# Kernel optimization log

Measured on AMD Instinct MI355X. Metric: run time of the kernel, lower is better.

The kernel has to match this reference:

```python
import jax, jax.numpy as jnp
import numpy as np
import math

SR = 96000.0
FRAME = 2048
NB = 16
GAIN_RANGE = (-24.0, 24.0)
Q_RANGE = (0.5, 16.0)
BROADBAND = (-60.0, 0.0)
HPF_R = (20.0, 500.0)
LPF_R = (5000.0, 20000.0)
SHELF_R = (50.0, 16000.0)
PEAK_R = (100.0, 15000.0)


def _dfreq(n, rng):
    lo, hi = math.log(rng[0]), math.log(rng[1])
    return jnp.exp(lo + n * (hi - lo))


def _dgain(n, rng=GAIN_RANGE):
    return rng[0] + n * (rng[1] - rng[0])


def _dq(n):
    lo, hi = math.log(Q_RANGE[0]), math.log(Q_RANGE[1])
    return jnp.exp(lo + n * (hi - lo))


def _coeffs(ftype, fc, gain_db, Q):
    # returns stacked [g, k, a1, a2, a3, m0, m1, m2], each same shape as fc
    g = jnp.clip(jnp.tan(math.pi * fc / SR), 1e-6, 100.0)
    Q = jnp.clip(Q, 0.1, 100.0)
    one = jnp.ones_like(g)
    zero = jnp.zeros_like(g)
    if ftype in ('highpass', 'lowpass'):
        k = 1.0 / Q
        a1 = 1.0 / (1.0 + g * (g + k)); a2 = g * a1; a3 = g * a2
        if ftype == 'highpass':
            m0, m1, m2 = one, -k, -one
        else:
            m0, m1, m2 = zero, zero, one
    elif ftype == 'peak':
        A = jnp.power(10.0, gain_db / 40.0)
        k = jnp.where(gain_db >= 0, 1.0 / (Q * A), A / Q)
        a1 = 1.0 / (1.0 + g * (g + k)); a2 = g * a1; a3 = g * a2
        m0, m1, m2 = one, k * (A * A - 1.0), zero
    elif ftype == 'lowshelf':
        A = jnp.power(10.0, gain_db / 40.0); sA = jnp.sqrt(A); k = 1.0 / Q
        gs = jnp.where(gain_db >= 0, g / sA, g * sA)
        a1 = 1.0 / (1.0 + gs * (gs + k)); a2 = gs * a1; a3 = gs * a2
        m0, m1, m2 = one, k * (A - 1.0), A * A - 1.0
    else:  # highshelf
        A = jnp.power(10.0, gain_db / 40.0); sA = jnp.sqrt(A); k = 1.0 / Q
        gs = jnp.where(gain_db >= 0, g * sA, g / sA)
        a1 = 1.0 / (1.0 + gs * (gs + k)); a2 = gs * a1; a3 = gs * a2
        m0, m1, m2 = A * A, k * (1.0 - A) * A, 1.0 - A * A
    return jnp.stack([g, k, a1, a2, a3, m0, m1, m2], 0)


def _all_coeffs(params, n_frames_audio):
    # params: (B, 50, n_frames_params) -> coeffs (nF, NB, 8, B), in/out gains (nF, B)
    B = params.shape[0]
    nFp = params.shape[2]
    pidx = jnp.minimum(jnp.arange(n_frames_audio), nFp - 1)
    fp = jnp.take(params, pidx, axis=2)                 # (B, 50, nF)
    bq = fp[:, :NB * 3, :].reshape(B, NB, 3, n_frames_audio)
    in_g = jnp.power(10.0, _dgain(fp[:, -2, :], BROADBAND) / 20.0)   # (B, nF)
    out_g = jnp.power(10.0, _dgain(fp[:, -1, :], BROADBAND) / 20.0)  # (B, nF)
    cs = []
    for i in range(NB):
        fn, gn, qn = bq[:, i, 0], bq[:, i, 1], bq[:, i, 2]  # (B, nF)
        Q = _dq(qn)
        if i == 0:
            c = _coeffs('highpass', _dfreq(fn, HPF_R), None, Q)
        elif i == 15:
            c = _coeffs('lowpass', _dfreq(fn, LPF_R), None, Q)
        elif i == 1:
            c = _coeffs('lowshelf', _dfreq(fn, SHELF_R), _dgain(gn), Q)
        elif i == 14:
            c = _coeffs('highshelf', _dfreq(fn, SHELF_R), _dgain(gn), Q)
        else:
            c = _coeffs('peak', _dfreq(fn, PEAK_R), _dgain(gn), Q)
        cs.append(c)  # (8, B, nF)
    coeffs = jnp.transpose(jnp.stack(cs, 0), (3, 0, 1, 2))  # (nF, NB, 8, B)
    return coeffs, in_g.T, out_g.T


def _forward(audio, params):
    B, S = audio.shape
    nF = S // FRAME  # S chosen as exact multiple of FRAME
    coeffs, in_g, out_g = _all_coeffs(params, nF)
    frames = jnp.transpose(audio.reshape(B, nF, FRAME), (1, 2, 0))  # (nF, FRAME, B)

    def frame_step(states, xs):
        fr, c, ig, og = xs  # fr (FRAME,B), c (NB,8,B), ig (B,), og (B,)
        x = fr * ig[None, :]
        new_states = []
        for i in range(NB):
            a1, a2, a3 = c[i, 2], c[i, 3], c[i, 4]
            m0, m1, m2 = c[i, 5], c[i, 6], c[i, 7]

            def samp(st, xn, a1=a1, a2=a2, a3=a3, m0=m0, m1=m1, m2=m2):
                ic1, ic2 = st
                v3 = xn - ic2
                v1 = a1 * ic1 + a2 * v3
                v2 = ic2 + a2 * v1 + a3 * v3
                out = m0 * xn + m1 * v1 + m2 * v2
                return (2.0 * v1 - ic1, 2.0 * v2 - ic2), out

            (ic1, ic2), x = jax.lax.scan(samp, (states[i, 0], states[i, 1]), x)
            new_states.append(jnp.stack([ic1, ic2], 0))
        return jnp.stack(new_states, 0), x * og[None, :]

    init = jnp.zeros((NB, 2, B), audio.dtype)
    _, out = jax.lax.scan(frame_step, init, (frames, coeffs, in_g, out_g))
    return jnp.transpose(out, (2, 0, 1)).reshape(B, S)  # (B, S)


_forward_jit = jax.jit(_forward)


def setup_inputs() -> dict:
    key = jax.random.key(0)
    k1, k2 = jax.random.split(key)
    B, S, nFp = 32, 49152, 24  # 24 frames of 2048 samples
    audio = jax.random.normal(k1, (B, S), dtype=jnp.float32) * 0.1
    params = jax.random.uniform(k2, (B, 50, nFp), dtype=jnp.float32)
    return {'audio': audio, 'params': params}


def reference(audio, params):
    return _forward_jit(audio, params)
```

## Files before the change

kernel.cpp:

```cpp
#include <hip/hip_runtime.h>
#include <math.h>

#define NBATCH 32
#define S      49152
#define NF     24
#define NB     16
#define NBLK   4
#define CHUNK  16
#define NCH    768
#define NWAVE  12

__device__ __forceinline__ float clampf(float x, float lo, float hi) {
    return fminf(fmaxf(x, lo), hi);
}

#define FOREACH_S(OP) \
    OP(s00) OP(s01) OP(s02) OP(s03) OP(s04) OP(s05) OP(s06) OP(s07) \
    OP(s08) OP(s09) OP(s10) OP(s11) OP(s12) OP(s13) OP(s14) OP(s15)

#define DECL_S(x) float x;

#define STEPA(x) { \
    const float n1_ = fmaf(t00, ic1, fmaf(t01, ic2, b0 * (x))); \
    const float n2_ = fmaf(t10, ic1, fmaf(t11, ic2, b1 * (x))); \
    ic1 = n1_; ic2 = n2_; }

#define STEPC(x) { \
    const float y_  = fmaf(c0, ic1, fmaf(c1, ic2, c2 * (x))); \
    const float n1_ = fmaf(t00, ic1, fmaf(t01, ic2, b0 * (x))); \
    const float n2_ = fmaf(t10, ic1, fmaf(t11, ic2, b1 * (x))); \
    (x) = y_; ic1 = n1_; ic2 = n2_; }

__global__ __launch_bounds__(NCH, 3)
void biquad_chain_kernel(const float* __restrict__ audio,
                         const float* __restrict__ params,
                         float* __restrict__ out,
                         unsigned int* __restrict__ ws)
{
    __shared__ float sc[NB][NF][16];
    __shared__ float sgain[2][NF];
    __shared__ float4 saggM[NWAVE];
    __shared__ float  saggC[NWAVE][2];
    __shared__ float  sv[NWAVE][2];

    const int t       = threadIdx.x;
    const int xcd     = blockIdx.x & 7;
    const int slot_   = blockIdx.x >> 3;
    const int bt      = xcd * 4 + (slot_ & 3);
    const int quarter = slot_ >> 2;
    const int lane    = t & 63;
    const int wave    = t >> 6;
    const int frame   = quarter * 6 + (wave >> 1);

    if (t < NB * NF) {
        const int f  = t / NF;
        const int fr = t % NF;
        const float* P = params + (size_t)bt * 50 * NF;
        const float fn = P[(3 * f + 0) * NF + fr];
        const float gn = P[(3 * f + 1) * NF + fr];
        const float qn = P[(3 * f + 2) * NF + fr];

        float Q = __expf(-0.69314718f + qn * 3.4657359f);
        Q = clampf(Q, 0.1f, 100.0f);

        float lo, hi;
        int type;
        if      (f == 0)  { lo = 20.0f;   hi = 500.0f;   type = 0; }
        else if (f == 15) { lo = 5000.0f; hi = 20000.0f; type = 1; }
        else if (f == 1)  { lo = 50.0f;   hi = 16000.0f; type = 3; }
        else if (f == 14) { lo = 50.0f;   hi = 16000.0f; type = 4; }
        else              { lo = 100.0f;  hi = 15000.0f; type = 2; }

        const float fc = __expf(__logf(lo) + fn * (__logf(hi) - __logf(lo)));
        float g_ = __tanf((float)M_PI * fc / 96000.0f);
        g_ = clampf(g_, 1e-6f, 100.0f);
        const float gdb = -24.0f + 48.0f * gn;

        float a1, a2, a3, m0, m1, m2;
        if (type == 0 || type == 1) {
            const float k = 1.0f / Q;
            a1 = 1.0f / (1.0f + g_ * (g_ + k)); a2 = g_ * a1; a3 = g_ * a2;
            if (type == 0) { m0 = 1.0f; m1 = -k;   m2 = -1.0f; }
            else           { m0 = 0.0f; m1 = 0.0f; m2 = 1.0f;  }
        } else if (type == 2) {
            const float A = __expf(gdb * (2.30258509f / 40.0f));
            const float k = (gdb >= 0.0f) ? 1.0f / (Q * A) : A / Q;
            a1 = 1.0f / (1.0f + g_ * (g_ + k)); a2 = g_ * a1; a3 = g_ * a2;
            m0 = 1.0f; m1 = k * (A * A - 1.0f); m2 = 0.0f;
        } else {
            const float A  = __expf(gdb * (2.30258509f / 40.0f));
            const float sA = sqrtf(A);
            const float k  = 1.0f / Q;
            float gs;
            if (type == 3) gs = (gdb >= 0.0f) ? g_ / sA : g_ * sA;
            else           gs = (gdb >= 0.0f) ? g_ * sA : g_ / sA;
            a1 = 1.0f / (1.0f + gs * (gs + k)); a2 = gs * a1; a3 = gs * a2;
            if (type == 3) { m0 = 1.0f;  m1 = k * (A - 1.0f);      m2 = A * A - 1.0f; }
            else           { m0 = A * A; m1 = k * (1.0f - A) * A;  m2 = 1.0f - A * A; }
        }

        const float q2  = a2 * a2 + a3;
        const float t00 = 2.0f * a1 - 1.0f;
        const float t01 = -2.0f * a2;
        const float t10 = 2.0f * a1 * a2;
        const float t11 = 1.0f - 2.0f * q2;
        const float b0  = 2.0f * a2;
        const float b1  = 2.0f * q2;
        const float c0  = a1 * (m1 + m2 * a2);
        const float c1  = m2 * (1.0f - q2) - m1 * a2;
        const float c2  = m0 + m1 * a2 + m2 * q2;

        float u00 = t00, u01 = t01, u10 = t10, u11 = t11;
        #pragma unroll
        for (int i = 0; i < 4; i++) {
            const float n00 = u00 * u00 + u01 * u10;
            const float n01 = u00 * u01 + u01 * u11;
            const float n10 = u10 * u00 + u11 * u10;
            const float n11 = u10 * u01 + u11 * u11;
            u00 = n00; u01 = n01; u10 = n10; u11 = n11;
        }

        sc[f][fr][0] = t00; sc[f][fr][1] = t01; sc[f][fr][2] = t10; sc[f][fr][3] = t11;
        sc[f][fr][4] = b0;  sc[f][fr][5] = b1;  sc[f][fr][6] = c0;  sc[f][fr][7] = c1;
        sc[f][fr][8] = c2;  sc[f][fr][9] = u00; sc[f][fr][10] = u01; sc[f][fr][11] = u10;
        sc[f][fr][12] = u11;
    }
    if (t >= 384 && t < 384 + 2 * NF) {
        const int idx = t - 384;
        const int which = idx / NF;
        const int fr    = idx % NF;
        const float* P = params + (size_t)bt * 50 * NF;
        const float p  = P[(48 + which) * NF + fr];
        const float db = -60.0f + 60.0f * p;
        sgain[which][fr] = __expf(db * (2.30258509f / 20.0f));
    }
    __syncthreads();

    FOREACH_S(DECL_S)
    {
        const float ing = sgain[0][frame];
        const float* base = audio + (size_t)bt * S
                          + (size_t)(quarter * NCH + t) * CHUNK;
        float4 q;
        q = *(const float4*)(base +  0); s00 = q.x*ing; s01 = q.y*ing; s02 = q.z*ing; s03 = q.w*ing;
        q = *(const float4*)(base +  4); s04 = q.x*ing; s05 = q.y*ing; s06 = q.z*ing; s07 = q.w*ing;
        q = *(const float4*)(base +  8); s08 = q.x*ing; s09 = q.y*ing; s10 = q.z*ing; s11 = q.w*ing;
        q = *(const float4*)(base + 12); s12 = q.x*ing; s13 = q.y*ing; s14 = q.z*ing; s15 = q.w*ing;
    }

    #pragma unroll 1
    for (int f = 0; f < NB; f++) {
        const float4 q0 = *(const float4*)&sc[f][frame][0];
        const float4 q1 = *(const float4*)&sc[f][frame][4];
        const float4 q2 = *(const float4*)&sc[f][frame][8];
        const float  M11v = sc[f][frame][12];
        const float t00 = q0.x, t01 = q0.y, t10 = q0.z, t11 = q0.w;
        const float b0  = q1.x, b1  = q1.y, c0  = q1.z, c1  = q1.w;
        const float c2  = q2.x;

        float ic1 = 0.0f, ic2 = 0.0f;
        FOREACH_S(STEPA)

        float Md00 = q2.y, Md01 = q2.z, Md10 = q2.w, Md11 = M11v;
        float Ac0 = ic1, Ac1 = ic2;
        #pragma unroll
        for (int d = 1; d < 64; d <<= 1) {
            const float lc0 = __shfl_up(Ac0, d);
            const float lc1 = __shfl_up(Ac1, d);
            if (lane >= d) {
                Ac0 = fmaf(Md00, lc0, fmaf(Md01, lc1, Ac0));
                Ac1 = fmaf(Md10, lc0, fmaf(Md11, lc1, Ac1));
            }
            const float n00 = Md00 * Md00 + Md01 * Md10;
            const float n01 = Md00 * Md01 + Md01 * Md11;
            const float n10 = Md10 * Md00 + Md11 * Md10;
            const float n11 = Md10 * Md01 + Md11 * Md11;
            Md00 = n00; Md01 = n01; Md10 = n10; Md11 = n11;
        }

        if (lane == 63) {
            saggM[wave] = make_float4(Md00, Md01, Md10, Md11);
            saggC[wave][0] = Ac0; saggC[wave][1] = Ac1;
        }
        __syncthreads();

        const unsigned int tag = (unsigned int)(f + 1);
        unsigned int* stagebase = ws + ((bt * NB + f) * NBLK) * 8;

        if (wave == 0) {
            float G00 = 1.0f, G01 = 0.0f, G10 = 0.0f, G11 = 1.0f, Gc0 = 0.0f, Gc1 = 0.0f;
            if (lane < NWAVE) {
                const float4 m = saggM[lane];
                G00 = m.x; G01 = m.y; G10 = m.z; G11 = m.w;
                Gc0 = saggC[lane][0]; Gc1 = saggC[lane][1];
            }
            #pragma unroll
            for (int d = 1; d < 16; d <<= 1) {
                const float l00 = __shfl_up(G00, d);
                const float l01 = __shfl_up(G01, d);
                const float l10 = __shfl_up(G10, d);
                const float l11 = __shfl_up(G11, d);
                const float lc0 = __shfl_up(Gc0, d);
                const float lc1 = __shfl_up(Gc1, d);
                if (lane >= d && lane < NWAVE) {
                    const float n00 = G00 * l00 + G01 * l10;
                    const float n01 = G00 * l01 + G01 * l11;
                    const float n10 = G10 * l00 + G11 * l10;
                    const float n11 = G10 * l01 + G11 * l11;
                    const float nc0 = G00 * lc0 + G01 * lc1 + Gc0;
                    const float nc1 = G10 * lc0 + G11 * lc1 + Gc1;
                    G00 = n00; G01 = n01; G10 = n10; G11 = n11;
                    Gc0 = nc0; Gc1 = nc1;
                }
            }

            if (quarter < NBLK - 1 && lane == NWAVE - 1) {
                unsigned int* slot = stagebase + quarter * 8;
                float* dp = (float*)(slot + 1);
                __hip_atomic_store(&dp[0], G00, __ATOMIC_RELAXED, __HIP_MEMORY_SCOPE_AGENT);
                __hip_atomic_store(&dp[1], G01, __ATOMIC_RELAXED, __HIP_MEMORY_SCOPE_AGENT);
                __hip_atomic_store(&dp[2], G10, __ATOMIC_RELAXED, __HIP_MEMORY_SCOPE_AGENT);
                __hip_atomic_store(&dp[3], G11, __ATOMIC_RELAXED, __HIP_MEMORY_SCOPE_AGENT);
                __hip_atomic_store(&dp[4], Gc0, __ATOMIC_RELAXED, __HIP_MEMORY_SCOPE_AGENT);
                __hip_atomic_store(&dp[5], Gc1, __ATOMIC_RELAXED, __HIP_MEMORY_SCOPE_AGENT);
                __hip_atomic_store(slot, tag, __ATOMIC_RELEASE, __HIP_MEMORY_SCOPE_AGENT);
            }

            float P00 = __shfl_up(G00, 1);
            float P01 = __shfl_up(G01, 1);
            float P10 = __shfl_up(G10, 1);
            float P11 = __shfl_up(G11, 1);
            float Pc0 = __shfl_up(Gc0, 1);
            float Pc1 = __shfl_up(Gc1, 1);
            if (lane == 0) { P00 = 1.0f; P01 = 0.0f; P10 = 0.0f; P11 = 1.0f; Pc0 = 0.0f; Pc1 = 0.0f; }

            float S0x = 0.0f, S0y = 0.0f;
            if (lane == 0 && quarter > 0) {
                float sx = 0.0f, sy = 0.0f;
                for (int k2 = 0; k2 < quarter; k2++) {
                    unsigned int* slot = stagebase + k2 * 8;
                    while (__hip_atomic_load(slot, __ATOMIC_ACQUIRE, __HIP_MEMORY_SCOPE_AGENT) != tag) {
                        __builtin_amdgcn_s_sleep(1);
                    }
                    float* dp = (float*)(slot + 1);
                    const float m00 = __hip_atomic_load(&dp[0], __ATOMIC_RELAXED, __HIP_MEMORY_SCOPE_AGENT);
                    const float m01 = __hip_atomic_load(&dp[1], __ATOMIC_RELAXED, __HIP_MEMORY_SCOPE_AGENT);
                    const float m10 = __hip_atomic_load(&dp[2], __ATOMIC_RELAXED, __HIP_MEMORY_SCOPE_AGENT);
                    const float m11 = __hip_atomic_load(&dp[3], __ATOMIC_RELAXED, __HIP_MEMORY_SCOPE_AGENT);
                    const float cc0 = __hip_atomic_load(&dp[4], __ATOMIC_RELAXED, __HIP_MEMORY_SCOPE_AGENT);
                    const float cc1 = __hip_atomic_load(&dp[5], __ATOMIC_RELAXED, __HIP_MEMORY_SCOPE_AGENT);
                    const float nx = m00 * sx + m01 * sy + cc0;
                    const float ny = m10 * sx + m11 * sy + cc1;
                    sx = nx; sy = ny;
                }
                S0x = sx; S0y = sy;
            }
            S0x = __shfl(S0x, 0);
            S0y = __shfl(S0y, 0);

            if (lane < NWAVE) {
                sv[lane][0] = fmaf(P00, S0x, fmaf(P01, S0y, Pc0));
                sv[lane][1] = fmaf(P10, S0x, fmaf(P11, S0y, Pc1));
            }
        }
        __syncthreads();

        const float vx = sv[wave][0];
        const float vy = sv[wave][1];

        float ce0 = __shfl_up(Ac0, 1);
        float ce1 = __shfl_up(Ac1, 1);
        if (lane == 0) { ce0 = 0.0f; ce1 = 0.0f; }

        float w0 = vx, w1 = vy;
        float p00 = q2.y, p01 = q2.z, p10 = q2.w, p11 = M11v;
        #pragma unroll
        for (int b = 0; b < 6; b++) {
            if (lane & (1 << b)) {
                const float nw0 = fmaf(p00, w0, p01 * w1);
                const float nw1 = fmaf(p10, w0, p11 * w1);
                w0 = nw0; w1 = nw1;
            }
            if (b < 5) {
                const float n00 = p00 * p00 + p01 * p10;
                const float n01 = p00 * p01 + p01 * p11;
                const float n10 = p10 * p00 + p11 * p10;
                const float n11 = p10 * p01 + p11 * p11;
                p00 = n00; p01 = n01; p10 = n10; p11 = n11;
            }
        }
        ic1 = w0 + ce0;
        ic2 = w1 + ce1;

        FOREACH_S(STEPC)
    }

    {
        const float og = sgain[1][frame];
        float* base = out + (size_t)bt * S + (size_t)(quarter * NCH + t) * CHUNK;
        float4 q;
        q.x = s00*og; q.y = s01*og; q.z = s02*og; q.w = s03*og; *(float4*)(base +  0) = q;
        q.x = s04*og; q.y = s05*og; q.z = s06*og; q.w = s07*og; *(float4*)(base +  4) = q;
        q.x = s08*og; q.y = s09*og; q.z = s10*og; q.w = s11*og; *(float4*)(base +  8) = q;
        q.x = s12*og; q.y = s13*og; q.z = s14*og; q.w = s15*og; *(float4*)(base + 12) = q;
    }
}

extern "C" void kernel_launch(void* const* d_in, const int* in_sizes, int n_in,
                              void* d_out, int out_size, void* d_ws, size_t ws_size,
                              hipStream_t stream)
{
    const float* audio  = (const float*)d_in[0];
    const float* params = (const float*)d_in[1];
    float* out = (float*)d_out;
    unsigned int* ws = (unsigned int*)d_ws;
    biquad_chain_kernel<<<NBLK * NBATCH, NCH, 0, stream>>>(audio, params, out, ws);
}
```

Measured before the change: 125.3 us.

## Fuse biquad stages in pairs to halve parallel-scan and sync rounds

Result: slower. 204.6 us (+63.2%).

```diff
diff --git a/kernel.cpp b/kernel.cpp
--- a/kernel.cpp
+++ b/kernel.cpp
@@ -5,6 +5,7 @@
 #define S      49152
 #define NF     24
 #define NB     16
+#define NP     8
 #define NBLK   4
 #define CHUNK  16
 #define NCH    768
@@ -20,16 +21,82 @@
 
 #define DECL_S(x) float x;
 
-#define STEPA(x) { \
-    const float n1_ = fmaf(t00, ic1, fmaf(t01, ic2, b0 * (x))); \
-    const float n2_ = fmaf(t10, ic1, fmaf(t11, ic2, b1 * (x))); \
-    ic1 = n1_; ic2 = n2_; }
-
-#define STEPC(x) { \
-    const float y_  = fmaf(c0, ic1, fmaf(c1, ic2, c2 * (x))); \
-    const float n1_ = fmaf(t00, ic1, fmaf(t01, ic2, b0 * (x))); \
-    const float n2_ = fmaf(t10, ic1, fmaf(t11, ic2, b1 * (x))); \
-    (x) = y_; ic1 = n1_; ic2 = n2_; }
+#define STEPA2(x) { \
+    const float y1_  = fmaf(c0a, j1, fmaf(c1a, j2, c2a * (x))); \
+    const float nj1_ = fmaf(t00a, j1, fmaf(t01a, j2, b0a * (x))); \
+    const float nj2_ = fmaf(t10a, j1, fmaf(t11a, j2, b1a * (x))); \
+    const float nk1_ = fmaf(t00b, k1, fmaf(t01b, k2, b0b * y1_)); \
+    const float nk2_ = fmaf(t10b, k1, fmaf(t11b, k2, b1b * y1_)); \
+    j1 = nj1_; j2 = nj2_; k1 = nk1_; k2 = nk2_; }
+
+#define STEPC2(x) { \
+    const float y1_  = fmaf(c0a, j1, fmaf(c1a, j2, c2a * (x))); \
+    const float y2_  = fmaf(c0b, k1, fmaf(c1b, k2, c2b * y1_)); \
+    const float nj1_ = fmaf(t00a, j1, fmaf(t01a, j2, b0a * (x))); \
+    const float nj2_ = fmaf(t10a, j1, fmaf(t11a, j2, b1a * (x))); \
+    const float nk1_ = fmaf(t00b, k1, fmaf(t01b, k2, b0b * y1_)); \
+    const float nk2_ = fmaf(t10b, k1, fmaf(t11b, k2, b1b * y1_)); \
+    (x) = y2_; j1 = nj1_; j2 = nj2_; k1 = nk1_; k2 = nk2_; }
+
+struct Aff { float t00, t01, t10, t11, b0, b1, c0, c1, c2; };
+
+__device__ __forceinline__ Aff biquad_affine(int f, const float* P, int fr) {
+    const float fn = P[(3 * f + 0) * NF + fr];
+    const float gn = P[(3 * f + 1) * NF + fr];
+    const float qn = P[(3 * f + 2) * NF + fr];
+
+    float Q = __expf(-0.69314718f + qn * 3.4657359f);
+    Q = clampf(Q, 0.1f, 100.0f);
+
+    float lo, hi;
+    int type;
+    if      (f == 0)  { lo = 20.0f;   hi = 500.0f;   type = 0; }
+    else if (f == 15) { lo = 5000.0f; hi = 20000.0f; type = 1; }
+    else if (f == 1)  { lo = 50.0f;   hi = 16000.0f; type = 3; }
+    else if (f == 14) { lo = 50.0f;   hi = 16000.0f; type = 4; }
+    else              { lo = 100.0f;  hi = 15000.0f; type = 2; }
+
+    const float fc = __expf(__logf(lo) + fn * (__logf(hi) - __logf(lo)));
+    float g_ = __tanf((float)M_PI * fc / 96000.0f);
+    g_ = clampf(g_, 1e-6f, 100.0f);
+    const float gdb = -24.0f + 48.0f * gn;
+
+    float a1, a2, a3, m0, m1, m2;
+    if (type == 0 || type == 1) {
+        const float k = 1.0f / Q;
+        a1 = 1.0f / (1.0f + g_ * (g_ + k)); a2 = g_ * a1; a3 = g_ * a2;
+        if (type == 0) { m0 = 1.0f; m1 = -k;   m2 = -1.0f; }
+        else           { m0 = 0.0f; m1 = 0.0f; m2 = 1.0f;  }
+    } else if (type == 2) {
+        const float A = __expf(gdb * (2.30258509f / 40.0f));
+        const float k = (gdb >= 0.0f) ? 1.0f / (Q * A) : A / Q;
+        a1 = 1.0f / (1.0f + g_ * (g_ + k)); a2 = g_ * a1; a3 = g_ * a2;
+        m0 = 1.0f; m1 = k * (A * A - 1.0f); m2 = 0.0f;
+    } else {
+        const float A  = __expf(gdb * (2.30258509f / 40.0f));
+        const float sA = sqrtf(A);
+        const float k  = 1.0f / Q;
+        float gs;
+        if (type == 3) gs = (gdb >= 0.0f) ? g_ / sA : g_ * sA;
+        else           gs = (gdb >= 0.0f) ? g_ * sA : g_ / sA;
+        a1 = 1.0f / (1.0f + gs * (gs + k)); a2 = gs * a1; a3 = gs * a2;
+        if (type == 3) { m0 = 1.0f;  m1 = k * (A - 1.0f);      m2 = A * A - 1.0f; }
+        else           { m0 = A * A; m1 = k * (1.0f - A) * A;  m2 = 1.0f - A * A; }
+    }
+
+    const float q2 = a2 * a2 + a3;
+    Aff r;
+    r.t00 = 2.0f * a1 - 1.0f;
+    r.t01 = -2.0f * a2;
+    r.t10 = 2.0f * a1 * a2;
+    r.t11 = 1.0f - 2.0f * q2;
+    r.b0  = 2.0f * a2;
+    r.b1  = 2.0f * q2;
+    r.c0  = a1 * (m1 + m2 * a2);
+    r.c1  = m2 * (1.0f - q2) - m1 * a2;
+    r.c2  = m0 + m1 * a2 + m2 * q2;
+    return r;
+}
 
 __global__ __launch_bounds__(NCH, 3)
 void biquad_chain_kernel(const float* __restrict__ audio,
@@ -37,11 +104,10 @@
                          float* __restrict__ out,
                          unsigned int* __restrict__ ws)
 {
-    __shared__ float sc[NB][NF][16];
+    __shared__ float sc[NP][NF][32];
     __shared__ float sgain[2][NF];
-    __shared__ float4 saggM[NWAVE];
-    __shared__ float  saggC[NWAVE][2];
-    __shared__ float  sv[NWAVE][2];
+    __shared__ float sagg[NWAVE][16];
+    __shared__ float sv[NWAVE][4];
 
     const int t       = threadIdx.x;
     const int xcd     = blockIdx.x & 7;
@@ -52,78 +118,46 @@
     const int wave    = t >> 6;
     const int frame   = quarter * 6 + (wave >> 1);
 
-    if (t < NB * NF) {
-        const int f  = t / NF;
+    if (t < NP * NF) {
+        const int p  = t / NF;
         const int fr = t % NF;
         const float* P = params + (size_t)bt * 50 * NF;
-        const float fn = P[(3 * f + 0) * NF + fr];
-        const float gn = P[(3 * f + 1) * NF + fr];
-        const float qn = P[(3 * f + 2) * NF + fr];
-
-        float Q = __expf(-0.69314718f + qn * 3.4657359f);
-        Q = clampf(Q, 0.1f, 100.0f);
-
-        float lo, hi;
-        int type;
-        if      (f == 0)  { lo = 20.0f;   hi = 500.0f;   type = 0; }
-        else if (f == 15) { lo = 5000.0f; hi = 20000.0f; type = 1; }
-        else if (f == 1)  { lo = 50.0f;   hi = 16000.0f; type = 3; }
-        else if (f == 14) { lo = 50.0f;   hi = 16000.0f; type = 4; }
-        else              { lo = 100.0f;  hi = 15000.0f; type = 2; }
-
-        const float fc = __expf(__logf(lo) + fn * (__logf(hi) - __logf(lo)));
-        float g_ = __tanf((float)M_PI * fc / 96000.0f);
-        g_ = clampf(g_, 1e-6f, 100.0f);
-        const float gdb = -24.0f + 48.0f * gn;
-
-        float a1, a2, a3, m0, m1, m2;
-        if (type == 0 || type == 1) {
-            const float k = 1.0f / Q;
-            a1 = 1.0f / (1.0f + g_ * (g_ + k)); a2 = g_ * a1; a3 = g_ * a2;
-            if (type == 0) { m0 = 1.0f; m1 = -k;   m2 = -1.0f; }
-            else           { m0 = 0.0f; m1 = 0.0f; m2 = 1.0f;  }
-        } else if (type == 2) {
-            const float A = __expf(gdb * (2.30258509f / 40.0f));
-            const float k = (gdb >= 0.0f) ? 1.0f / (Q * A) : A / Q;
-            a1 = 1.0f / (1.0f + g_ * (g_ + k)); a2 = g_ * a1; a3 = g_ * a2;
-            m0 = 1.0f; m1 = k * (A * A - 1.0f); m2 = 0.0f;
-        } else {
-            const float A  = __expf(gdb * (2.30258509f / 40.0f));
-            const float sA = sqrtf(A);
-            const float k  = 1.0f / Q;
-            float gs;
-            if (type == 3) gs = (gdb >= 0.0f) ? g_ / sA : g_ * sA;
-            else           gs = (gdb >= 0.0f) ? g_ * sA : g_ / sA;
-            a1 = 1.0f / (1.0f + gs * (gs + k)); a2 = gs * a1; a3 = gs * a2;
-            if (type == 3) { m0 = 1.0f;  m1 = k * (A - 1.0f);      m2 = A * A - 1.0f; }
-            else           { m0 = A * A; m1 = k * (1.0f - A) * A;  m2 = 1.0f - A * A; }
-        }
-
-        const float q2  = a2 * a2 + a3;
-        const float t00 = 2.0f * a1 - 1.0f;
-        const float t01 = -2.0f * a2;
-        const float t10 = 2.0f * a1 * a2;
-        const float t11 = 1.0f - 2.0f * q2;
-        const float b0  = 2.0f * a2;
-        const float b1  = 2.0f * q2;
-        const float c0  = a1 * (m1 + m2 * a2);
-        const float c1  = m2 * (1.0f - q2) - m1 * a2;
-        const float c2  = m0 + m1 * a2 + m2 * q2;
-
-        float u00 = t00, u01 = t01, u10 = t10, u11 = t11;
+        const Aff A = biquad_affine(2 * p,     P, fr);
+        const Aff B = biquad_affine(2 * p + 1, P, fr);
+
+        float a00 = A.t00, a01 = A.t01, a10 = A.t10, a11 = A.t11;
+        float x00 = B.b0 * A.c0, x01 = B.b0 * A.c1;
+        float x10 = B.b1 * A.c0, x11 = B.b1 * A.c1;
+        float b00 = B.t00, b01 = B.t01, b10 = B.t10, b11 = B.t11;
+
         #pragma unroll
         for (int i = 0; i < 4; i++) {
-            const float n00 = u00 * u00 + u01 * u10;
-            const float n01 = u00 * u01 + u01 * u11;
-            const float n10 = u10 * u00 + u11 * u10;
-            const float n11 = u10 * u01 + u11 * u11;
-            u00 = n00; u01 = n01; u10 = n10; u11 = n11;
+            const float na00 = a00 * a00 + a01 * a10;
+            const float na01 = a00 * a01 + a01 * a11;
+            const float na10 = a10 * a00 + a11 * a10;
+            const float na11 = a10 * a01 + a11 * a11;
+            const float nx00 = x00 * a00 + x01 * a10 + b00 * x00 + b01 * x10;
+            const float nx01 = x00 * a01 + x01 * a11 + b00 * x01 + b01 * x11;
+            const float nx10 = x10 * a00 + x11 * a10 + b10 * x00 + b11 * x10;
+            const float nx11 = x10 * a01 + x11 * a11 + b10 * x01 + b11 * x11;
+            const float nb00 = b00 * b00 + b01 * b10;
+            const float nb01 = b00 * b01 + b01 * b11;
+            const float nb10 = b10 * b00 + b11 * b10;
+            const float nb11 = b10 * b01 + b11 * b11;
+            a00 = na00; a01 = na01; a10 = na10; a11 = na11;
+            x00 = nx00; x01 = nx01; x10 = nx10; x11 = nx11;
+            b00 = nb00; b01 = nb01; b10 = nb10; b11 = nb11;
         }
 
-        sc[f][fr][0] = t00; sc[f][fr][1] = t01; sc[f][fr][2] = t10; sc[f][fr][3] = t11;
-        sc[f][fr][4] = b0;  sc[f][fr][5] = b1;  sc[f][fr][6] = c0;  sc[f][fr][7] = c1;
-        sc[f][fr][8] = c2;  sc[f][fr][9] = u00; sc[f][fr][10] = u01; sc[f][fr][11] = u10;
-        sc[f][fr][12] = u11;
+        float* d = sc[p][fr];
+        d[0]  = A.t00; d[1]  = A.t01; d[2]  = A.t10; d[3]  = A.t11;
+        d[4]  = A.b0;  d[5]  = A.b1;  d[6]  = A.c0;  d[7]  = A.c1;
+        d[8]  = A.c2;  d[9]  = B.t00; d[10] = B.t01; d[11] = B.t10;
+        d[12] = B.t11; d[13] = B.b0;  d[14] = B.b1;  d[15] = B.c0;
+        d[16] = B.c1;  d[17] = B.c2;  d[18] = a00;   d[19] = a01;
+        d[20] = a10;   d[21] = a11;   d[22] = x00;   d[23] = x01;
+        d[24] = x10;   d[25] = x11;   d[26] = b00;   d[27] = b01;
+        d[28] = b10;   d[29] = b11;   d[30] = 0.0f;  d[31] = 0.0f;
     }
     if (t >= 384 && t < 384 + 2 * NF) {
         const int idx = t - 384;
@@ -149,150 +183,253 @@
     }
 
     #pragma unroll 1
-    for (int f = 0; f < NB; f++) {
-        const float4 q0 = *(const float4*)&sc[f][frame][0];
-        const float4 q1 = *(const float4*)&sc[f][frame][4];
-        const float4 q2 = *(const float4*)&sc[f][frame][8];
-        const float  M11v = sc[f][frame][12];
-        const float t00 = q0.x, t01 = q0.y, t10 = q0.z, t11 = q0.w;
-        const float b0  = q1.x, b1  = q1.y, c0  = q1.z, c1  = q1.w;
-        const float c2  = q2.x;
-
-        float ic1 = 0.0f, ic2 = 0.0f;
-        FOREACH_S(STEPA)
-
-        float Md00 = q2.y, Md01 = q2.z, Md10 = q2.w, Md11 = M11v;
-        float Ac0 = ic1, Ac1 = ic2;
+    for (int f = 0; f < NP; f++) {
+        const float* d = sc[f][frame];
+        const float4 q0 = *(const float4*)(d +  0);
+        const float4 q1 = *(const float4*)(d +  4);
+        const float4 q2 = *(const float4*)(d +  8);
+        const float4 q3 = *(const float4*)(d + 12);
+        const float4 q4 = *(const float4*)(d + 16);
+        const float4 q5 = *(const float4*)(d + 20);
+        const float4 q6 = *(const float4*)(d + 24);
+        const float4 q7 = *(const float4*)(d + 28);
+        const float t00a = q0.x, t01a = q0.y, t10a = q0.z, t11a = q0.w;
+        const float b0a  = q1.x, b1a  = q1.y, c0a  = q1.z, c1a  = q1.w;
+        const float c2a  = q2.x, t00b = q2.y, t01b = q2.z, t10b = q2.w;
+        const float t11b = q3.x, b0b  = q3.y, b1b  = q3.z, c0b  = q3.w;
+        const float c1b  = q4.x, c2b  = q4.y;
+        const float M11_00 = q4.z, M11_01 = q4.w;
+        const float M11_10 = q5.x, M11_11 = q5.y;
+        const float M21_00 = q5.z, M21_01 = q5.w;
+        const float M21_10 = q6.x, M21_11 = q6.y;
+        const float M22_00 = q6.z, M22_01 = q6.w;
+        const float M22_10 = q7.x, M22_11 = q7.y;
+
+        float j1 = 0.0f, j2 = 0.0f, k1 = 0.0f, k2 = 0.0f;
+        FOREACH_S(STEPA2)
+
+        float m11_00 = M11_00, m11_01 = M11_01, m11_10 = M11_10, m11_11 = M11_11;
+        float m21_00 = M21_00, m21_01 = M21_01, m21_10 = M21_10, m21_11 = M21_11;
+        float m22_00 = M22_00, m22_01 = M22_01, m22_10 = M22_10, m22_11 = M22_11;
+        float Ac1 = j1, Ac2 = j2, Ac3 = k1, Ac4 = k2;
         #pragma unroll
-        for (int d = 1; d < 64; d <<= 1) {
-            const float lc0 = __shfl_up(Ac0, d);
-            const float lc1 = __shfl_up(Ac1, d);
-            if (lane >= d) {
-                Ac0 = fmaf(Md00, lc0, fmaf(Md01, lc1, Ac0));
-                Ac1 = fmaf(Md10, lc0, fmaf(Md11, lc1, Ac1));
-            }
-            const float n00 = Md00 * Md00 + Md01 * Md10;
-            const float n01 = Md00 * Md01 + Md01 * Md11;
-            const float n10 = Md10 * Md00 + Md11 * Md10;
-            const float n11 = Md10 * Md01 + Md11 * Md11;
-            Md00 = n00; Md01 = n01; Md10 = n10; Md11 = n11;
+        for (int dd = 1; dd < 64; dd <<= 1) {
+            const float l1 = __shfl_up(Ac1, dd);
+            const float l2 = __shfl_up(Ac2, dd);
+            const float l3 = __shfl_up(Ac3, dd);
+            const float l4 = __shfl_up(Ac4, dd);
+            if (lane >= dd) {
+                const float n1 = fmaf(m11_00, l1, fmaf(m11_01, l2, Ac1));
+                const float n2 = fmaf(m11_10, l1, fmaf(m11_11, l2, Ac2));
+                const float n3 = fmaf(m21_00, l1, fmaf(m21_01, l2, fmaf(m22_00, l3, fmaf(m22_01, l4, Ac3))));
+                const float n4 = fmaf(m21_10, l1, fmaf(m21_11, l2, fmaf(m22_10, l3, fmaf(m22_11, l4, Ac4))));
+                Ac1 = n1; Ac2 = n2; Ac3 = n3; Ac4 = n4;
+            }
+            const float na00 = m11_00 * m11_00 + m11_01 * m11_10;
+            const float na01 = m11_00 * m11_01 + m11_01 * m11_11;
+            const float na10 = m11_10 * m11_00 + m11_11 * m11_10;
+            const float na11 = m11_10 * m11_01 + m11_11 * m11_11;
+            const float nx00 = m21_00 * m11_00 + m21_01 * m11_10 + m22_00 * m21_00 + m22_01 * m21_10;
+            const float nx01 = m21_00 * m11_01 + m21_01 * m11_11 + m22_00 * m21_01 + m22_01 * m21_11;
+            const float nx10 = m21_10 * m11_00 + m21_11 * m11_10 + m22_10 * m21_00 + m22_11 * m21_10;
+            const float nx11 = m21_10 * m11_01 + m21_11 * m11_11 + m22_10 * m21_01 + m22_11 * m21_11;
+            const float nb00 = m22_00 * m22_00 + m22_01 * m22_10;
+            const float nb01 = m22_00 * m22_01 + m22_01 * m22_11;
+            const float nb10 = m22_10 * m22_00 + m22_11 * m22_10;
+            const float nb11 = m22_10 * m22_01 + m22_11 * m22_11;
+            m11_00 = na00; m11_01 = na01; m11_10 = na10; m11_11 = na11;
+            m21_00 = nx00; m21_01 = nx01; m21_10 = nx10; m21_11 = nx11;
+            m22_00 = nb00; m22_01 = nb01; m22_10 = nb10; m22_11 = nb11;
         }
 
         if (lane == 63) {
-            saggM[wave] = make_float4(Md00, Md01, Md10, Md11);
-            saggC[wave][0] = Ac0; saggC[wave][1] = Ac1;
+            float* g = sagg[wave];
+            g[0]  = m11_00; g[1]  = m11_01; g[2]  = m11_10; g[3]  = m11_11;
+            g[4]  = m21_00; g[5]  = m21_01; g[6]  = m21_10; g[7]  = m21_11;
+            g[8]  = m22_00; g[9]  = m22_01; g[10] = m22_10; g[11] = m22_11;
+            g[12] = Ac1;    g[13] = Ac2;    g[14] = Ac3;    g[15] = Ac4;
         }
         __syncthreads();
 
         const unsigned int tag = (unsigned int)(f + 1);
-        unsigned int* stagebase = ws + ((bt * NB + f) * NBLK) * 8;
+        unsigned int* stagebase = ws + ((size_t)(bt * NP + f) * NBLK) * 20;
 
         if (wave == 0) {
-            float G00 = 1.0f, G01 = 0.0f, G10 = 0.0f, G11 = 1.0f, Gc0 = 0.0f, Gc1 = 0.0f;
+            float g11_00 = 1.0f, g11_01 = 0.0f, g11_10 = 0.0f, g11_11 = 1.0f;
+            float g21_00 = 0.0f, g21_01 = 0.0f, g21_10 = 0.0f, g21_11 = 0.0f;
+            float g22_00 = 1.0f, g22_01 = 0.0f, g22_10 = 0.0f, g22_11 = 1.0f;
+            float gc1 = 0.0f, gc2 = 0.0f, gc3 = 0.0f, gc4 = 0.0f;
             if (lane < NWAVE) {
-                const float4 m = saggM[lane];
-                G00 = m.x; G01 = m.y; G10 = m.z; G11 = m.w;
-                Gc0 = saggC[lane][0]; Gc1 = saggC[lane][1];
+                const float* g = sagg[lane];
+                g11_00 = g[0];  g11_01 = g[1];  g11_10 = g[2];  g11_11 = g[3];
+                g21_00 = g[4];  g21_01 = g[5];  g21_10 = g[6];  g21_11 = g[7];
+                g22_00 = g[8];  g22_01 = g[9];  g22_10 = g[10]; g22_11 = g[11];
+                gc1 = g[12]; gc2 = g[13]; gc3 = g[14]; gc4 = g[15];
             }
             #pragma unroll
-            for (int d = 1; d < 16; d <<= 1) {
-                const float l00 = __shfl_up(G00, d);
-                const float l01 = __shfl_up(G01, d);
-                const float l10 = __shfl_up(G10, d);
-                const float l11 = __shfl_up(G11, d);
-                const float lc0 = __shfl_up(Gc0, d);
-                const float lc1 = __shfl_up(Gc1, d);
-                if (lane >= d && lane < NWAVE) {
-                    const float n00 = G00 * l00 + G01 * l10;
-                    const float n01 = G00 * l01 + G01 * l11;
-                    const float n10 = G10 * l00 + G11 * l10;
-                    const float n11 = G10 * l01 + G11 * l11;
-                    const float nc0 = G00 * lc0 + G01 * lc1 + Gc0;
-                    const float nc1 = G10 * lc0 + G11 * lc1 + Gc1;
-                    G00 = n00; G01 = n01; G10 = n10; G11 = n11;
-                    Gc0 = nc0; Gc1 = nc1;
+            for (int dd = 1; dd < 16; dd <<= 1) {
+                const float L11_00 = __shfl_up(g11_00, dd), L11_01 = __shfl_up(g11_01, dd);
+                const float L11_10 = __shfl_up(g11_10, dd), L11_11 = __shfl_up(g11_11, dd);
+                const float L21_00 = __shfl_up(g21_00, dd), L21_01 = __shfl_up(g21_01, dd);
+                const float L21_10 = __shfl_up(g21_10, dd), L21_11 = __shfl_up(g21_11, dd);
+                const float L22_00 = __shfl_up(g22_00, dd), L22_01 = __shfl_up(g22_01, dd);
+                const float L22_10 = __shfl_up(g22_10, dd), L22_11 = __shfl_up(g22_11, dd);
+                const float lc1 = __shfl_up(gc1, dd), lc2 = __shfl_up(gc2, dd);
+                const float lc3 = __shfl_up(gc3, dd), lc4 = __shfl_up(gc4, dd);
+                if (lane >= dd && lane < NWAVE) {
+                    const float n11_00 = g11_00 * L11_00 + g11_01 * L11_10;
+                    const float n11_01 = g11_00 * L11_01 + g11_01 * L11_11;
+                    const float n11_10 = g11_10 * L11_00 + g11_11 * L11_10;
+                    const float n11_11 = g11_10 * L11_01 + g11_11 * L11_11;
+                    const float n21_00 = g21_00 * L11_00 + g21_01 * L11_10 + g22_00 * L21_00 + g22_01 * L21_10;
+                    const float n21_01 = g21_00 * L11_01 + g21_01 * L11_11 + g22_00 * L21_01 + g22_01 * L21_11;
+                    const float n21_10 = g21_10 * L11_00 + g21_11 * L11_10 + g22_10 * L21_00 + g22_11 * L21_10;
+                    const float n21_11 = g21_10 * L11_01 + g21_11 * L11_11 + g22_10 * L21_01 + g22_11 * L21_11;
+                    const float n22_00 = g22_00 * L22_00 + g22_01 * L22_10;
+                    const float n22_01 = g22_00 * L22_01 + g22_01 * L22_11;
+                    const float n22_10 = g22_10 * L22_00 + g22_11 * L22_10;
+                    const float n22_11 = g22_10 * L22_01 + g22_11 * L22_11;
+                    const float nc1 = fmaf(g11_00, lc1, fmaf(g11_01, lc2, gc1));
+                    const float nc2 = fmaf(g11_10, lc1, fmaf(g11_11, lc2, gc2));
+                    const float nc3 = fmaf(g21_00, lc1, fmaf(g21_01, lc2, fmaf(g22_00, lc3, fmaf(g22_01, lc4, gc3))));
+                    const float nc4 = fmaf(g21_10, lc1, fmaf(g21_11, lc2, fmaf(g22_10, lc3, fmaf(g22_11, lc4, gc4))));
+                    g11_00 = n11_00; g11_01 = n11_01; g11_10 = n11_10; g11_11 = n11_11;
+                    g21_00 = n21_00; g21_01 = n21_01; g21_10 = n21_10; g21_11 = n21_11;
+                    g22_00 = n22_00; g22_01 = n22_01; g22_10 = n22_10; g22_11 = n22_11;
+                    gc1 = nc1; gc2 = nc2; gc3 = nc3; gc4 = nc4;
                 }
             }
 
             if (quarter < NBLK - 1 && lane == NWAVE - 1) {
-                unsigned int* slot = stagebase + quarter * 8;
+                unsigned int* slot = stagebase + quarter * 20;
                 float* dp = (float*)(slot + 1);
-                __hip_atomic_store(&dp[0], G00, __ATOMIC_RELAXED, __HIP_MEMORY_SCOPE_AGENT);
-                __hip_atomic_store(&dp[1], G01, __ATOMIC_RELAXED, __HIP_MEMORY_SCOPE_AGENT);
-                __hip_atomic_store(&dp[2], G10, __ATOMIC_RELAXED, __HIP_MEMORY_SCOPE_AGENT);
-                __hip_atomic_store(&dp[3], G11, __ATOMIC_RELAXED, __HIP_MEMORY_SCOPE_AGENT);
-                __hip_atomic_store(&dp[4], Gc0, __ATOMIC_RELAXED, __HIP_MEMORY_SCOPE_AGENT);
-                __hip_atomic_store(&dp[5], Gc1, __ATOMIC_RELAXED, __HIP_MEMORY_SCOPE_AGENT);
+                __hip_atomic_store(&dp[0],  g11_00, __ATOMIC_RELAXED, __HIP_MEMORY_SCOPE_AGENT);
+                __hip_atomic_store(&dp[1],  g11_01, __ATOMIC_RELAXED, __HIP_MEMORY_SCOPE_AGENT);
+                __hip_atomic_store(&dp[2],  g11_10, __ATOMIC_RELAXED, __HIP_MEMORY_SCOPE_AGENT);
+                __hip_atomic_store(&dp[3],  g11_11, __ATOMIC_RELAXED, __HIP_MEMORY_SCOPE_AGENT);
+                __hip_atomic_store(&dp[4],  g21_00, __ATOMIC_RELAXED, __HIP_MEMORY_SCOPE_AGENT);
+                __hip_atomic_store(&dp[5],  g21_01, __ATOMIC_RELAXED, __HIP_MEMORY_SCOPE_AGENT);
+                __hip_atomic_store(&dp[6],  g21_10, __ATOMIC_RELAXED, __HIP_MEMORY_SCOPE_AGENT);
+                __hip_atomic_store(&dp[7],  g21_11, __ATOMIC_RELAXED, __HIP_MEMORY_SCOPE_AGENT);
+                __hip_atomic_store(&dp[8],  g22_00, __ATOMIC_RELAXED, __HIP_MEMORY_SCOPE_AGENT);
+                __hip_atomic_store(&dp[9],  g22_01, __ATOMIC_RELAXED, __HIP_MEMORY_SCOPE_AGENT);
+                __hip_atomic_store(&dp[10], g22_10, __ATOMIC_RELAXED, __HIP_MEMORY_SCOPE_AGENT);
+                __hip_atomic_store(&dp[11], g22_11, __ATOMIC_RELAXED, __HIP_MEMORY_SCOPE_AGENT);
+                __hip_atomic_store(&dp[12], gc1,    __ATOMIC_RELAXED, __HIP_MEMORY_SCOPE_AGENT);
+                __hip_atomic_store(&dp[13], gc2,    __ATOMIC_RELAXED, __HIP_MEMORY_SCOPE_AGENT);
+                __hip_atomic_store(&dp[14], gc3,    __ATOMIC_RELAXED, __HIP_MEMORY_SCOPE_AGENT);
+                __hip_atomic_store(&dp[15], gc4,    __ATOMIC_RELAXED, __HIP_MEMORY_SCOPE_AGENT);
                 __hip_atomic_store(slot, tag, __ATOMIC_RELEASE, __HIP_MEMORY_SCOPE_AGENT);
             }
 
-            float P00 = __shfl_up(G00, 1);
-            float P01 = __shfl_up(G01, 1);
-            float P10 = __shfl_up(G10, 1);
-            float P11 = __shfl_up(G11, 1);
-            float Pc0 = __shfl_up(Gc0, 1);
-            float Pc1 = __shfl_up(Gc1, 1);
-            if (lane == 0) { P00 = 1.0f; P01 = 0.0f; P10 = 0.0f; P11 = 1.0f; Pc0 = 0.0f; Pc1 = 0.0f; }
-
-            float S0x = 0.0f, S0y = 0.0f;
+            float p11_00 = __shfl_up(g11_00, 1), p11_01 = __shfl_up(g11_01, 1);
+            float p11_10 = __shfl_up(g11_10, 1), p11_11 = __shfl_up(g11_11, 1);
+            float p21_00 = __shfl_up(g21_00, 1), p21_01 = __shfl_up(g21_01, 1);
+            float p21_10 = __shfl_up(g21_10, 1), p21_11 = __shfl_up(g21_11, 1);
+            float p22_00 = __shfl_up(g22_00, 1), p22_01 = __shfl_up(g22_01, 1);
+            float p22_10 = __shfl_up(g22_10, 1), p22_11 = __shfl_up(g22_11, 1);
+            float pc1 = __shfl_up(gc1, 1), pc2 = __shfl_up(gc2, 1);
+            float pc3 = __shfl_up(gc3, 1), pc4 = __shfl_up(gc4, 1);
+            if (lane == 0) {
+                p11_00 = 1.0f; p11_01 = 0.0f; p11_10 = 0.0f; p11_11 = 1.0f;
+                p21_00 = 0.0f; p21_01 = 0.0f; p21_10 = 0.0f; p21_11 = 0.0f;
+                p22_00 = 1.0f; p22_01 = 0.0f; p22_10 = 0.0f; p22_11 = 1.0f;
+                pc1 = 0.0f; pc2 = 0.0f; pc3 = 0.0f; pc4 = 0.0f;
+            }
+
+            float S1 = 0.0f, S2 = 0.0f, S3 = 0.0f, S4 = 0.0f;
             if (lane == 0 && quarter > 0) {
-                float sx = 0.0f, sy = 0.0f;
-                for (int k2 = 0; k2 < quarter; k2++) {
-                    unsigned int* slot = stagebase + k2 * 8;
+                float s1 = 0.0f, s2 = 0.0f, s3 = 0.0f, s4 = 0.0f;
+                for (int kq = 0; kq < quarter; kq++) {
+                    unsigned int* slot = stagebase + kq * 20;
                     while (__hip_atomic_load(slot, __ATOMIC_ACQUIRE, __HIP_MEMORY_SCOPE_AGENT) != tag) {
                         __builtin_amdgcn_s_sleep(1);
                     }
-                    float* dp = (float*)(slot + 1);
-                    const float m00 = __hip_atomic_load(&dp[0], __ATOMIC_RELAXED, __HIP_MEMORY_SCOPE_AGENT);
-                    const float m01 = __hip_atomic_load(&dp[1], __ATOMIC_RELAXED, __HIP_MEMORY_SCOPE_AGENT);
-                    const float m10 = __hip_atomic_load(&dp[2], __ATOMIC_RELAXED, __HIP_MEMORY_SCOPE_AGENT);
-                    const float m11 = __hip_atomic_load(&dp[3], __ATOMIC_RELAXED, __HIP_MEMORY_SCOPE_AGENT);
-                    const float cc0 = __hip_atomic_load(&dp[4], __ATOMIC_RELAXED, __HIP_MEMORY_SCOPE_AGENT);
-                    const float cc1 = __hip_atomic_load(&dp[5], __ATOMIC_RELAXED, __HIP_MEMORY_SCOPE_AGENT);
-                    const float nx = m00 * sx + m01 * sy + cc0;
-                    const float ny = m10 * sx + m11 * sy + cc1;
-                    sx = nx; sy = ny;
+                    const float* dp = (const float*)(slot + 1);
+                    const float a00 = __hip_atomic_load(&dp[0],  __ATOMIC_RELAXED, __HIP_MEMORY_SCOPE_AGENT);
+                    const float a01 = __hip_atomic_load(&dp[1],  __ATOMIC_RELAXED, __HIP_MEMORY_SCOPE_AGENT);
+                    const float a10 = __hip_atomic_load(&dp[2],  __ATOMIC_RELAXED, __HIP_MEMORY_SCOPE_AGENT);
+                    const float a11 = __hip_atomic_load(&dp[3],  __ATOMIC_RELAXED, __HIP_MEMORY_SCOPE_AGENT);
+                    const float x00 = __hip_atomic_load(&dp[4],  __ATOMIC_RELAXED, __HIP_MEMORY_SCOPE_AGENT);
+                    const float x01 = __hip_atomic_load(&dp[5],  __ATOMIC_RELAXED, __HIP_MEMORY_SCOPE_AGENT);
+                    const float x10 = __hip_atomic_load(&dp[6],  __ATOMIC_RELAXED, __HIP_MEMORY_SCOPE_AGENT);
+                    const float x11 = __hip_atomic_load(&dp[7],  __ATOMIC_RELAXED, __HIP_MEMORY_SCOPE_AGENT);
+                    const float e00 = __hip_atomic_load(&dp[8],  __ATOMIC_RELAXED, __HIP_MEMORY_SCOPE_AGENT);
+                    const float e01 = __hip_atomic_load(&dp[9],  __ATOMIC_RELAXED, __HIP_MEMORY_SCOPE_AGENT);
+                    const float e10 = __hip_atomic_load(&dp[10], __ATOMIC_RELAXED, __HIP_MEMORY_SCOPE_AGENT);
+                    const float e11 = __hip_atomic_load(&dp[11], __ATOMIC_RELAXED, __HIP_MEMORY_SCOPE_AGENT);
+                    const float cc1 = __hip_atomic_load(&dp[12], __ATOMIC_RELAXED, __HIP_MEMORY_SCOPE_AGENT);
+                    const float cc2 = __hip_atomic_load(&dp[13], __ATOMIC_RELAXED, __HIP_MEMORY_SCOPE_AGENT);
+                    const float cc3 = __hip_atomic_load(&dp[14], __ATOMIC_RELAXED, __HIP_MEMORY_SCOPE_AGENT);
+                    const float cc4 = __hip_atomic_load(&dp[15], __ATOMIC_RELAXED, __HIP_MEMORY_SCOPE_AGENT);
+                    const float n1 = fmaf(a00, s1, fmaf(a01, s2, cc1));
+                    const float n2 = fmaf(a10, s1, fmaf(a11, s2, cc2));
+                    const float n3 = fmaf(x00, s1, fmaf(x01, s2, fmaf(e00, s3, fmaf(e01, s4, cc3))));
+                    const float n4 = fmaf(x10, s1, fmaf(x11, s2, fmaf(e10, s3, fmaf(e11, s4, cc4))));
+                    s1 = n1; s2 = n2; s3 = n3; s4 = n4;
                 }
-                S0x = sx; S0y = sy;
-            }
-            S0x = __shfl(S0x, 0);
-            S0y = __shfl(S0y, 0);
+                S1 = s1; S2 = s2; S3 = s3; S4 = s4;
+            }
+            S1 = __shfl(S1, 0); S2 = __shfl(S2, 0);
+            S3 = __shfl(S3, 0); S4 = __shfl(S4, 0);
 
             if (lane < NWAVE) {
-                sv[lane][0] = fmaf(P00, S0x, fmaf(P01, S0y, Pc0));
-                sv[lane][1] = fmaf(P10, S0x, fmaf(P11, S0y, Pc1));
+                sv[lane][0] = fmaf(p11_00, S1, fmaf(p11_01, S2, pc1));
+                sv[lane][1] = fmaf(p11_10, S1, fmaf(p11_11, S2, pc2));
+                sv[lane][2] = fmaf(p21_00, S1, fmaf(p21_01, S2, fmaf(p22_00, S3, fmaf(p22_01, S4, pc3))));
+                sv[lane][3] = fmaf(p21_10, S1, fmaf(p21_11, S2, fmaf(p22_10, S3, fmaf(p22_11, S4, pc4))));
             }
         }
         __syncthreads();
 
-        const float vx = sv[wave][0];
-        const float vy = sv[wave][1];
-
-        float ce0 = __shfl_up(Ac0, 1);
+        const float vx1 = sv[wave][0];
+        const float vx2 = sv[wave][1];
+        const float vx3 = sv[wave][2];
+        const float vx4 = sv[wave][3];
+
         float ce1 = __shfl_up(Ac1, 1);
-        if (lane == 0) { ce0 = 0.0f; ce1 = 0.0f; }
-
-        float w0 = vx, w1 = vy;
-        float p00 = q2.y, p01 = q2.z, p10 = q2.w, p11 = M11v;
+        float ce2 = __shfl_up(Ac2, 1);
+        float ce3 = __shfl_up(Ac3, 1);
+        float ce4 = __shfl_up(Ac4, 1);
+        if (lane == 0) { ce1 = 0.0f; ce2 = 0.0f; ce3 = 0.0f; ce4 = 0.0f; }
+
+        float w1 = vx1, w2 = vx2, w3 = vx3, w4 = vx4;
+        float pa00 = M11_00, pa01 = M11_01, pa10 = M11_10, pa11 = M11_11;
+        float px00 = M21_00, px01 = M21_01, px10 = M21_10, px11 = M21_11;
+        float pb00 = M22_00, pb01 = M22_01, pb10 = M22_10, pb11 = M22_11;
         #pragma unroll
         for (int b = 0; b < 6; b++) {
             if (lane & (1 << b)) {
-                const float nw0 = fmaf(p00, w0, p01 * w1);
-                const float nw1 = fmaf(p10, w0, p11 * w1);
-                w0 = nw0; w1 = nw1;
+                const float n1 = pa00 * w1 + pa01 * w2;
+                const float n2 = pa10 * w1 + pa11 * w2;
+                const float n3 = px00 * w1 + px01 * w2 + pb00 * w3 + pb01 * w4;
+                const float n4 = px10 * w1 + px11 * w2 + pb10 * w3 + pb11 * w4;
+                w1 = n1; w2 = n2; w3 = n3; w4 = n4;
             }
             if (b < 5) {
-                const float n00 = p00 * p00 + p01 * p10;
-                const float n01 = p00 * p01 + p01 * p11;
-                const float n10 = p10 * p00 + p11 * p10;
-                const float n11 = p10 * p01 + p11 * p11;
-                p00 = n00; p01 = n01; p10 = n10; p11 = n11;
+                const float na00 = pa00 * pa00 + pa01 * pa10;
+                const float na01 = pa00 * pa01 + pa01 * pa11;
+                const float na10 = pa10 * pa00 + pa11 * pa10;
+                const float na11 = pa10 * pa01 + pa11 * pa11;
+                const float nx00 = px00 * pa00 + px01 * pa10 + pb00 * px00 + pb01 * px10;
+                const float nx01 = px00 * pa01 + px01 * pa11 + pb00 * px01 + pb01 * px11;
+                const float nx10 = px10 * pa00 + px11 * pa10 + pb10 * px00 + pb11 * px10;
+                const float nx11 = px10 * pa01 + px11 * pa11 + pb10 * px01 + pb11 * px11;
+                const float nb00 = pb00 * pb00 + pb01 * pb10;
+                const float nb01 = pb00 * pb01 + pb01 * pb11;
+                const float nb10 = pb10 * pb00 + pb11 * pb10;
+                const float nb11 = pb10 * pb01 + pb11 * pb11;
+                pa00 = na00; pa01 = na01; pa10 = na10; pa11 = na11;
+                px00 = nx00; px01 = nx01; px10 = nx10; px11 = nx11;
+                pb00 = nb00; pb01 = nb01; pb10 = nb10; pb11 = nb11;
             }
         }
-        ic1 = w0 + ce0;
-        ic2 = w1 + ce1;
-
-        FOREACH_S(STEPC)
+        j1 = w1 + ce1;
+        j2 = w2 + ce2;
+        k1 = w3 + ce3;
+        k2 = w4 + ce4;
+
+        FOREACH_S(STEPC2)
     }
 
     {
```
